# Kernel optimization log

Measured on AMD Instinct MI355X. Metric: run time of the kernel, lower is better.

## Reference

```python
import jax, jax.numpy as jnp
import numpy as np
from jax import lax

DH = 256   # d_hidden
NL = 8     # number of wavenet cells
K = 3      # kernel_size
DIN = 16   # d_lag + d_cov
DOUT = 1
T, B = 1024, 64


def setup_inputs() -> dict:
    key = jax.random.key(0)
    ks = jax.random.split(key, 20)
    s = 0.05
    inp = {
        "X_emb": jax.random.randint(ks[0], (T, B, 1), 0, 10),
        "X_cov": jax.random.normal(ks[1], (T, B, 8), jnp.float32),
        "X_lag": jax.random.normal(ks[2], (T, B, 8), jnp.float32),
        "y": jax.random.normal(ks[3], (T, B, DOUT), jnp.float32),
        "domain": jax.random.uniform(ks[4], (B, 4), jnp.float32),
        "up_w": jax.random.normal(ks[5], (DIN, DH), jnp.float32) * s,
        "up_b": jnp.zeros((DH,), jnp.float32),
        "conv_dil_w": jax.random.normal(ks[6], (NL, 2 * DH, DH, K), jnp.float32) * s,
        "conv_dil_b": jnp.zeros((NL, 2 * DH), jnp.float32),
        "skip_w": jax.random.normal(ks[7], (NL, 2 * DH, DH), jnp.float32) * s,
        "skip_b": jnp.zeros((NL, 2 * DH), jnp.float32),
        "fc_w": jax.random.normal(ks[8], (DH, DH), jnp.float32) * s,
        "fc_b": jnp.zeros((DH,), jnp.float32),
        "loc_w": jax.random.normal(ks[9], (DH, DOUT), jnp.float32) * s,
        "loc_b": jnp.zeros((DOUT,), jnp.float32),
        "scale_w": jax.random.normal(ks[10], (DH, DOUT), jnp.float32) * s,
        "scale_b": jnp.zeros((DOUT,), jnp.float32),
        "d_outputseqlen": 24,
    }
    return inp


def _causal_conv(h, w, b, dil):
    # h: [B, C, T], w: [O, C, K] -> causal (left-padded) dilated conv
    pad = (w.shape[-1] - 1) * dil
    y = lax.conv_general_dilated(h, w, window_strides=(1,), padding=[(pad, 0)],
                                 rhs_dilation=(dil,),
                                 dimension_numbers=("NCH", "OIH", "NCH"))
    return y + b[None, :, None]


def _forward(X_cov, X_lag, y, up_w, up_b, conv_dil_w, conv_dil_b,
             skip_w, skip_b, fc_w, fc_b, loc_w, loc_b, scale_w, scale_b,
             d_outputseqlen):
    t = X_lag.shape[0]
    h = jnp.concatenate([X_lag, X_cov[:t]], axis=-1) @ up_w + up_b  # [T,B,DH]
    h = jnp.transpose(h, (1, 2, 0))  # [B, DH, T]
    skip = jnp.zeros_like(h)
    for i in range(NL):
        fg = _causal_conv(h, conv_dil_w[i], conv_dil_b[i], 2 ** i)  # [B,2DH,T]
        f, g = jnp.split(fg, 2, axis=1)
        gated = jnp.tanh(f) * jax.nn.sigmoid(g)  # [B,DH,T]
        hs = jnp.einsum("oc,bct->bot", skip_w[i], gated) + skip_b[i][None, :, None]
        h_next, skip_next = jnp.split(hs, 2, axis=1)
        h = h + h_next
        skip = skip + skip_next
    feat = jnp.transpose(skip, (2, 0, 1))  # [T,B,DH]
    ff = jax.nn.relu(feat @ fc_w + fc_b)
    tail = ff[-d_outputseqlen:]
    loc = tail @ loc_w + loc_b
    scale = jax.nn.softplus(tail @ scale_w + scale_b) + 1e-6
    yt = y[-d_outputseqlen:]
    log_prob = (-0.5 * ((yt - loc) / scale) ** 2
                - jnp.log(scale) - 0.5 * np.log(2.0 * np.pi))
    loss_y = -jnp.mean(log_prob)
    total_loss = loss_y  # loss_d forced to 0 in the original forward
    return total_loss, loss_y, loc, scale


def reference(X_emb, X_cov, X_lag, y, domain, up_w, up_b, conv_dil_w,
              conv_dil_b, skip_w, skip_b, fc_w, fc_b, loc_w, loc_b,
              scale_w, scale_b, d_outputseqlen):
    # X_emb and domain are unused with d_emb=[] and loss_d hard-set to 0.
    return _forward(X_cov, X_lag, y, up_w, up_b, conv_dil_w, conv_dil_b,
                    skip_w, skip_b, fc_w, fc_b, loc_w, loc_b,
                    scale_w, scale_b, d_outputseqlen)
```

## Files before the change

kernel.cpp:

```cpp
#include <hip/hip_runtime.h>
#include <math.h>

static constexpr int TT = 1024, BB = 64, DHID = 256, NLAY = 8, OSL = 24;

typedef __attribute__((ext_vector_type(8))) short short8;
typedef __attribute__((ext_vector_type(4))) float f32x4;
typedef unsigned short u16;
typedef __attribute__((ext_vector_type(4))) unsigned short u16x4;
typedef unsigned int u32;

__device__ __forceinline__ u16 f2bf(float x) {
  u32 u = __float_as_uint(x);
  return (u16)((u + 0x7fffu + ((u >> 16) & 1u)) >> 16);
}

__device__ __forceinline__ void gll16(const u16* g, u16* l) {
  __builtin_amdgcn_global_load_lds((const __attribute__((address_space(1))) void*)g,
                                   (__attribute__((address_space(3))) void*)l, 16, 0, 0);
}

__global__ __launch_bounds__(256) void wprep(
    const float* __restrict__ cw, const float* __restrict__ sw,
    u16* __restrict__ wT, u16* __restrict__ swT)
{
  const int stride = gridDim.x * 256;
  for (int idx = blockIdx.x * 256 + threadIdx.x; idx < NLAY * 3 * 512 * 256; idx += stride) {
    const int c = idx & 255;
    const int o = (idx >> 8) & 511;
    const int lt = idx >> 17;
    const int tap = lt % 3, l = lt / 3;
    wT[idx] = f2bf(cw[((size_t)(l * 512 + o) * 256 + c) * 3 + tap]);
  }
  for (int idx = blockIdx.x * 256 + threadIdx.x; idx < NLAY * 512 * 256; idx += stride)
    swT[idx] = f2bf(sw[idx]);
}

__global__ __launch_bounds__(256) void up_kernel(
    const float* __restrict__ xlag, const float* __restrict__ xcov,
    const float* __restrict__ upw, const float* __restrict__ upb,
    float* __restrict__ h, u16* __restrict__ hb0)
{
  const int b  = blockIdx.y;
  const int t0 = blockIdx.x * 16;
  __shared__ float xs[16][17];
  {
    const int tl = threadIdx.x >> 4;
    const int j  = threadIdx.x & 15;
    const size_t base = ((size_t)(t0 + tl) * BB + b) * 8;
    xs[tl][j] = (j < 8) ? xlag[base + j] : xcov[base + (j - 8)];
  }
  __syncthreads();
  const int c = threadIdx.x;
  float uw[16];
#pragma unroll
  for (int j = 0; j < 16; ++j) uw[j] = upw[j * DHID + c];
  const float bias = upb[c];
#pragma unroll
  for (int tl = 0; tl < 16; ++tl) {
    float acc = bias;
#pragma unroll
    for (int j = 0; j < 16; ++j) acc = fmaf(xs[tl][j], uw[j], acc);
    const size_t idx = ((size_t)b * TT + t0 + tl) * DHID + c;
    h[idx]   = acc;
    hb0[idx] = f2bf(acc);
  }
}

__global__ __launch_bounds__(512, 4) void layer_fused(
    const u16* __restrict__ hbin, const u16* __restrict__ wT,
    const float* __restrict__ cb, const u16* __restrict__ swT,
    const float* __restrict__ sb, float* __restrict__ hf,
    u16* __restrict__ hbout, float* __restrict__ skipf,
    const int dil, const int tile0)
{
  __shared__ u16 As[512 * 32];
  __shared__ u16 Bs[64 * 32];
  __shared__ u16 gLDS[64 * 264];

  const int b    = blockIdx.y;
  const int tile = tile0 + blockIdx.x;
  const int t0   = tile * 64;
  const bool last = (tile == 15);
  const int tid = threadIdx.x, w = tid >> 6, lane = tid & 63;
  const int l16 = lane & 15, quad = lane >> 4;
  const u16* hb = hbin + (size_t)b * TT * DHID;

  f32x4 acc[4][4];
  const f32x4 zero = {0.f, 0.f, 0.f, 0.f};
#pragma unroll
  for (int m = 0; m < 4; ++m)
#pragma unroll
    for (int n = 0; n < 4; ++n) acc[m][n] = zero;

  for (int tap = 0; tap < 3; ++tap) {
    const int sh = (2 - tap) * dil;
    const u16* wtap = wT + (size_t)tap * 512 * 256;
    for (int kc = 0; kc < 8; ++kc) {
      const int c0 = kc * 32;
#pragma unroll
      for (int q = 0; q < 4; ++q) {
        const int lin = q * 512 + tid;
        gll16(wtap + (size_t)(lin >> 2) * 256 + c0 + (lin & 3) * 8,
              As + (size_t)(q * 512 + (tid & ~63)) * 8);
      }
      if (w < 4) {
        const int tl = 16 * w + (lane >> 2);
        gll16(hb + (size_t)(t0 - sh + tl) * 256 + c0 + (lane & 3) * 8,
              Bs + w * 512);
      }
      __syncthreads();
      short8 bfr[4], afr[4];
#pragma unroll
      for (int nt = 0; nt < 4; ++nt)
        bfr[nt] = *(const short8*)&Bs[(nt * 16 + l16) * 32 + quad * 8];
#pragma unroll
      for (int m = 0; m < 4; ++m) {
        const int o = ((m & 2) ? 256 : 0) + 32 * w + (m & 1) * 16 + l16;
        afr[m] = *(const short8*)&As[(size_t)o * 32 + quad * 8];
      }
#pragma unroll
      for (int m = 0; m < 4; ++m)
#pragma unroll
        for (int nt = 0; nt < 4; ++nt)
          acc[m][nt] = __builtin_amdgcn_mfma_f32_16x16x32_bf16(afr[m], bfr[nt], acc[m][nt], 0, 0, 0);
      __syncthreads();
    }
  }

#pragma unroll
  for (int mf = 0; mf < 2; ++mf) {
#pragma unroll
    for (int nt = 0; nt < 4; ++nt) {
      u16x4 pk;
#pragma unroll
      for (int r = 0; r < 4; ++r) {
        const int c = 32 * w + mf * 16 + quad * 4 + r;
        const float f = acc[mf][nt][r] + cb[c];
        const float g = acc[mf + 2][nt][r] + cb[256 + c];
        const float th = 2.f / (1.f + __expf(-2.f * f)) - 1.f;
        const float sg = 1.f / (1.f + __expf(-g));
        pk[r] = f2bf(th * sg);
      }
      *(u16x4*)&gLDS[(size_t)(nt * 16 + l16) * 264 + 32 * w + mf * 16 + quad * 4] = pk;
    }
  }
  __syncthreads();

#pragma unroll
  for (int m = 0; m < 4; ++m)
#pragma unroll
    for (int n = 0; n < 4; ++n) acc[m][n] = zero;

  const int nq = last ? 4 : 2;
  for (int kc = 0; kc < 8; ++kc) {
    const int c0 = kc * 32;
    for (int q = 0; q < nq; ++q) {
      const int lin = q * 512 + tid;
      gll16(swT + (size_t)(lin >> 2) * 256 + c0 + (lin & 3) * 8,
            As + (size_t)(q * 512 + (tid & ~63)) * 8);
    }
    __syncthreads();
    short8 bfr[4];
#pragma unroll
    for (int nt = 0; nt < 4; ++nt)
      bfr[nt] = *(const short8*)&gLDS[(size_t)(nt * 16 + l16) * 264 + c0 + quad * 8];
#pragma unroll
    for (int m = 0; m < 2; ++m) {
      const int o = 32 * w + m * 16 + l16;
      short8 a = *(const short8*)&As[(size_t)o * 32 + quad * 8];
#pragma unroll
      for (int nt = 0; nt < 4; ++nt)
        acc[m][nt] = __builtin_amdgcn_mfma_f32_16x16x32_bf16(a, bfr[nt], acc[m][nt], 0, 0, 0);
    }
    if (last) {
#pragma unroll
      for (int m = 2; m < 4; ++m) {
        const int o = 256 + 32 * w + (m & 1) * 16 + l16;
        short8 a = *(const short8*)&As[(size_t)o * 32 + quad * 8];
#pragma unroll
        for (int nt = 0; nt < 4; ++nt)
          acc[m][nt] = __builtin_amdgcn_mfma_f32_16x16x32_bf16(a, bfr[nt], acc[m][nt], 0, 0, 0);
      }
    }
    __syncthreads();
  }

#pragma unroll
  for (int mh = 0; mh < 2; ++mh) {
#pragma unroll
    for (int nt = 0; nt < 4; ++nt) {
      const int t  = t0 + nt * 16 + l16;
      const int c4 = 32 * w + mh * 16 + quad * 4;
      const size_t idx = ((size_t)b * TT + t) * DHID + c4;
      f32x4 hv = *(f32x4*)&hf[idx];
      u16x4 pk;
#pragma unroll
      for (int r = 0; r < 4; ++r) {
        const float v = hv[r] + acc[mh][nt][r] + sb[c4 + r];
        hv[r] = v;
        pk[r] = f2bf(v);
      }
      *(f32x4*)&hf[idx] = hv;
      *(u16x4*)&hbout[idx] = pk;
    }
  }
  if (last) {
#pragma unroll
    for (int mh = 0; mh < 2; ++mh) {
#pragma unroll
      for (int nt = 0; nt < 4; ++nt) {
        const int tl = nt * 16 + l16;
        const int c4 = 32 * w + mh * 16 + quad * 4;
        const size_t idx = ((size_t)b * 64 + tl) * DHID + c4;
        f32x4 sv = *(f32x4*)&skipf[idx];
#pragma unroll
        for (int r = 0; r < 4; ++r)
          sv[r] += acc[mh + 2][nt][r] + sb[256 + c4 + r];
        *(f32x4*)&skipf[idx] = sv;
      }
    }
  }
}

__global__ __launch_bounds__(256) void head_kernel(
    const float* __restrict__ skipf,
    const float* __restrict__ fcw, const float* __restrict__ fcb,
    const float* __restrict__ locw, const float* __restrict__ locb,
    const float* __restrict__ scw, const float* __restrict__ scb,
    float* __restrict__ out)
{
  const int tt = blockIdx.x;
  const int b  = blockIdx.y;
  const int tl = 40 + tt;
  const int c  = threadIdx.x;
  __shared__ float xs[DHID];
  xs[c] = skipf[((size_t)b * 64 + tl) * DHID + c];
  __syncthreads();
  float acc = fcb[c];
#pragma unroll 8
  for (int j = 0; j < DHID; ++j) acc = fmaf(xs[j], fcw[j * DHID + c], acc);
  const float ff = fmaxf(acc, 0.f);
  float pl = ff * locw[c];
  float ps = ff * scw[c];
#pragma unroll
  for (int off = 32; off > 0; off >>= 1) {
    pl += __shfl_down(pl, off);
    ps += __shfl_down(ps, off);
  }
  __shared__ float rl[4], rs[4];
  const int wid = threadIdx.x >> 6, lane = threadIdx.x & 63;
  if (lane == 0) { rl[wid] = pl; rs[wid] = ps; }
  __syncthreads();
  if (threadIdx.x == 0) {
    const float loc = rl[0] + rl[1] + rl[2] + rl[3] + locb[0];
    const float x   = rs[0] + rs[1] + rs[2] + rs[3] + scb[0];
    const float sp  = (x > 0.f) ? (x + log1pf(expf(-x))) : log1pf(expf(x));
    out[2 + tt * BB + b]            = loc;
    out[2 + OSL * BB + tt * BB + b] = sp + 1e-6f;
  }
}

__global__ __launch_bounds__(256) void loss_kernel(
    const float* __restrict__ y, float* __restrict__ out)
{
  float s = 0.f;
  for (int i = threadIdx.x; i < OSL * BB; i += 256) {
    const int tt = i >> 6, b = i & 63;
    const float loc = out[2 + i];
    const float sc  = out[2 + OSL * BB + i];
    const float yt  = y[(size_t)(TT - OSL + tt) * BB + b];
    const float z   = (yt - loc) / sc;
    s += -0.5f * z * z - logf(sc) - 0.9189385332046727f;
  }
#pragma unroll
  for (int off = 32; off > 0; off >>= 1) s += __shfl_down(s, off);
  __shared__ float r[4];
  if ((threadIdx.x & 63) == 0) r[threadIdx.x >> 6] = s;
  __syncthreads();
  if (threadIdx.x == 0) {
    const float loss = -(r[0] + r[1] + r[2] + r[3]) / (float)(OSL * BB);
    out[0] = loss;
    out[1] = loss;
  }
}

extern "C" void kernel_launch(void* const* d_in, const int* in_sizes, int n_in,
                              void* d_out, int out_size, void* d_ws, size_t ws_size,
                              hipStream_t stream) {
  (void)in_sizes; (void)n_in; (void)out_size; (void)ws_size;
  const float* X_cov  = (const float*)d_in[1];
  const float* X_lag  = (const float*)d_in[2];
  const float* y      = (const float*)d_in[3];
  const float* up_w   = (const float*)d_in[5];
  const float* up_b   = (const float*)d_in[6];
  const float* conv_w = (const float*)d_in[7];
  const float* conv_b = (const float*)d_in[8];
  const float* skip_w = (const float*)d_in[9];
  const float* skip_b = (const float*)d_in[10];
  const float* fc_w   = (const float*)d_in[11];
  const float* fc_b   = (const float*)d_in[12];
  const float* loc_w  = (const float*)d_in[13];
  const float* loc_b  = (const float*)d_in[14];
  const float* sc_w   = (const float*)d_in[15];
  const float* sc_b   = (const float*)d_in[16];

  float* hf    = (float*)d_ws;
  u16*   hb0   = (u16*)  ((char*)d_ws + 67108864);
  u16*   hb1   = (u16*)  ((char*)d_ws + 100663296);
  float* skipf = (float*)((char*)d_ws + 134217728);
  u16*   wT    = (u16*)  ((char*)d_ws + 138412032);
  u16*   swT   = (u16*)  ((char*)d_ws + 144703488);

  wprep<<<2048, 256, 0, stream>>>(conv_w, skip_w, wT, swT);
  hipMemsetAsync(skipf, 0, (size_t)BB * 64 * DHID * sizeof(float), stream);
  up_kernel<<<dim3(TT / 16, BB), 256, 0, stream>>>(X_lag, X_cov, up_w, up_b, hf, hb0);

  static const int Ptab[NLAY] = {4, 5, 6, 7, 8, 9, 11, 15};
  u16* hin = hb0;
  u16* hout = hb1;
  for (int i = 0; i < NLAY; ++i) {
    const int ntiles = 16 - Ptab[i];
    layer_fused<<<dim3(ntiles, BB), 512, 0, stream>>>(
        hin, wT + (size_t)i * 3 * 512 * 256, conv_b + i * 512,
        swT + (size_t)i * 512 * 256, skip_b + i * 512,
        hf, hout, skipf, 1 << i, Ptab[i]);
    u16* tmp = hin; hin = hout; hout = tmp;
  }

  head_kernel<<<dim3(OSL, BB), 256, 0, stream>>>(
      skipf, fc_w, fc_b, loc_w, loc_b, sc_w, sc_b, (float*)d_out);
  loss_kernel<<<1, 256, 0, stream>>>(y, (float*)d_out);
}
```

Measured before the change: 734.3 us.

## Double-buffer layer GEMM with two batches per 1024-thread block

The fused layer kernel now processes two batch elements per 1024-thread block, so each staged weight tile is reused across 128 time positions instead of 64. LDS staging is double-buffered across the 24 conv steps and the 8 skip steps, which removes one barrier per step and overlaps loads with MFMA work. The up-projection kernel also skips the first 192 timesteps, which the receptive-field pruning of the later layers never reads. The larger blocks cut occupancy and raise LDS use per block, and the grid has half as many blocks.

```diff
diff --git a/kernel.cpp b/kernel.cpp
--- a/kernel.cpp
+++ b/kernel.cpp
@@ -41,7 +41,7 @@
     float* __restrict__ h, u16* __restrict__ hb0)
 {
   const int b  = blockIdx.y;
-  const int t0 = blockIdx.x * 16;
+  const int t0 = 192 + blockIdx.x * 16;
   __shared__ float xs[16][17];
   {
     const int tl = threadIdx.x >> 4;
@@ -66,156 +66,172 @@
   }
 }
 
-__global__ __launch_bounds__(512, 4) void layer_fused(
+__global__ __launch_bounds__(1024) void layer_fused(
     const u16* __restrict__ hbin, const u16* __restrict__ wT,
-    const float* __restrict__ cb, const u16* __restrict__ swT,
+    const float* __restrict__ cb, const u16* __restrict__ swTl,
     const float* __restrict__ sb, float* __restrict__ hf,
     u16* __restrict__ hbout, float* __restrict__ skipf,
     const int dil, const int tile0)
 {
-  __shared__ u16 As[512 * 32];
-  __shared__ u16 Bs[64 * 32];
-  __shared__ u16 gLDS[64 * 264];
-
-  const int b    = blockIdx.y;
+  __shared__ u16 As[2][2048 * 8];
+  __shared__ u16 Bs[2][512 * 8];
+  __shared__ u16 gS[4096 * 8];
+
+  const int b0   = blockIdx.y * 2;
   const int tile = tile0 + blockIdx.x;
   const int t0   = tile * 64;
   const bool last = (tile == 15);
-  const int tid = threadIdx.x, w = tid >> 6, lane = tid & 63;
+  const int tid = threadIdx.x;
+  const int w = tid >> 6, lane = tid & 63;
   const int l16 = lane & 15, quad = lane >> 4;
-  const u16* hb = hbin + (size_t)b * TT * DHID;
-
-  f32x4 acc[4][4];
+  const u16* hbB = hbin + (size_t)b0 * TT * DHID;
+
+  f32x4 acc[2][8];
   const f32x4 zero = {0.f, 0.f, 0.f, 0.f};
 #pragma unroll
-  for (int m = 0; m < 4; ++m)
-#pragma unroll
-    for (int n = 0; n < 4; ++n) acc[m][n] = zero;
-
-  for (int tap = 0; tap < 3; ++tap) {
+  for (int m = 0; m < 2; ++m)
+#pragma unroll
+    for (int n = 0; n < 8; ++n) acc[m][n] = zero;
+
+  auto stageConv = [&](int buf, int tap, int kc) {
     const int sh = (2 - tap) * dil;
+    const int c0 = kc * 32;
     const u16* wtap = wT + (size_t)tap * 512 * 256;
-    for (int kc = 0; kc < 8; ++kc) {
-      const int c0 = kc * 32;
-#pragma unroll
-      for (int q = 0; q < 4; ++q) {
-        const int lin = q * 512 + tid;
-        gll16(wtap + (size_t)(lin >> 2) * 256 + c0 + (lin & 3) * 8,
-              As + (size_t)(q * 512 + (tid & ~63)) * 8);
-      }
-      if (w < 4) {
-        const int tl = 16 * w + (lane >> 2);
-        gll16(hb + (size_t)(t0 - sh + tl) * 256 + c0 + (lane & 3) * 8,
-              Bs + w * 512);
-      }
-      __syncthreads();
-      short8 bfr[4], afr[4];
-#pragma unroll
-      for (int nt = 0; nt < 4; ++nt)
-        bfr[nt] = *(const short8*)&Bs[(nt * 16 + l16) * 32 + quad * 8];
-#pragma unroll
-      for (int m = 0; m < 4; ++m) {
-        const int o = ((m & 2) ? 256 : 0) + 32 * w + (m & 1) * 16 + l16;
-        afr[m] = *(const short8*)&As[(size_t)o * 32 + quad * 8];
-      }
-#pragma unroll
-      for (int m = 0; m < 4; ++m)
-#pragma unroll
-        for (int nt = 0; nt < 4; ++nt)
-          acc[m][nt] = __builtin_amdgcn_mfma_f32_16x16x32_bf16(afr[m], bfr[nt], acc[m][nt], 0, 0, 0);
-      __syncthreads();
-    }
-  }
-
-#pragma unroll
-  for (int mf = 0; mf < 2; ++mf) {
-#pragma unroll
-    for (int nt = 0; nt < 4; ++nt) {
+#pragma unroll
+    for (int q = 0; q < 2; ++q) {
+      const int s = q * 1024 + tid;
+      const int p = s >> 9, o = s & 511;
+      gll16(wtap + (size_t)o * 256 + c0 + p * 8, As[buf] + (size_t)(s & ~63) * 8);
+    }
+    if (tid < 512) {
+      const int s = tid;
+      const int p = s >> 7, tp = s & 127;
+      gll16(hbB + ((size_t)(tp >> 6) * TT + (t0 - sh + (tp & 63))) * 256 + c0 + p * 8,
+            Bs[buf] + (size_t)(s & ~63) * 8);
+    }
+  };
+  auto stageSkip = [&](int buf, int kc) {
+    const int c0 = kc * 32;
+    if (!last) {
+      const int s = tid;
+      const int p = s >> 8, o = s & 255;
+      gll16(swTl + (size_t)o * 256 + c0 + p * 8, As[buf] + (size_t)(s & ~63) * 8);
+    } else {
+#pragma unroll
+      for (int q = 0; q < 2; ++q) {
+        const int s = q * 1024 + tid;
+        const int p = s >> 9, o = s & 511;
+        gll16(swTl + (size_t)o * 256 + c0 + p * 8, As[buf] + (size_t)(s & ~63) * 8);
+      }
+    }
+  };
+
+  stageConv(0, 0, 0);
+  __syncthreads();
+  for (int step = 0; step < 24; ++step) {
+    const int ns = step + 1;
+    if (ns < 24) stageConv(ns & 1, ns >> 3, ns & 7);
+    else         stageSkip(0, 0);
+    const u16* A = As[step & 1];
+    const u16* B = Bs[step & 1];
+    const short8 af0 = *(const short8*)&A[(size_t)(quad * 512 + 16 * w + l16) * 8];
+    const short8 af1 = *(const short8*)&A[(size_t)(quad * 512 + 256 + 16 * w + l16) * 8];
+#pragma unroll
+    for (int half = 0; half < 2; ++half) {
+      short8 bf[4];
+#pragma unroll
+      for (int j = 0; j < 4; ++j)
+        bf[j] = *(const short8*)&B[(size_t)(quad * 128 + 16 * (4 * half + j) + l16) * 8];
+#pragma unroll
+      for (int j = 0; j < 4; ++j) {
+        const int nt = 4 * half + j;
+        acc[0][nt] = __builtin_amdgcn_mfma_f32_16x16x32_bf16(af0, bf[j], acc[0][nt], 0, 0, 0);
+        acc[1][nt] = __builtin_amdgcn_mfma_f32_16x16x32_bf16(af1, bf[j], acc[1][nt], 0, 0, 0);
+      }
+    }
+    __syncthreads();
+  }
+
+  {
+    const int cpart = 2 * w + (quad >> 1);
+    const int e0 = 4 * (quad & 1);
+#pragma unroll
+    for (int nt = 0; nt < 8; ++nt) {
+      const int tp = 16 * nt + l16;
       u16x4 pk;
 #pragma unroll
       for (int r = 0; r < 4; ++r) {
-        const int c = 32 * w + mf * 16 + quad * 4 + r;
-        const float f = acc[mf][nt][r] + cb[c];
-        const float g = acc[mf + 2][nt][r] + cb[256 + c];
+        const int c = 16 * w + 4 * quad + r;
+        const float f = acc[0][nt][r] + cb[c];
+        const float g = acc[1][nt][r] + cb[256 + c];
         const float th = 2.f / (1.f + __expf(-2.f * f)) - 1.f;
         const float sg = 1.f / (1.f + __expf(-g));
         pk[r] = f2bf(th * sg);
       }
-      *(u16x4*)&gLDS[(size_t)(nt * 16 + l16) * 264 + 32 * w + mf * 16 + quad * 4] = pk;
-    }
-  }
-  __syncthreads();
-
-#pragma unroll
-  for (int m = 0; m < 4; ++m)
-#pragma unroll
-    for (int n = 0; n < 4; ++n) acc[m][n] = zero;
-
-  const int nq = last ? 4 : 2;
-  for (int kc = 0; kc < 8; ++kc) {
-    const int c0 = kc * 32;
-    for (int q = 0; q < nq; ++q) {
-      const int lin = q * 512 + tid;
-      gll16(swT + (size_t)(lin >> 2) * 256 + c0 + (lin & 3) * 8,
-            As + (size_t)(q * 512 + (tid & ~63)) * 8);
+      *(u16x4*)&gS[((size_t)cpart * 128 + tp) * 8 + e0] = pk;
+    }
+  }
+  __syncthreads();
+
+#pragma unroll
+  for (int m = 0; m < 2; ++m)
+#pragma unroll
+    for (int n = 0; n < 8; ++n) acc[m][n] = zero;
+
+  const int aStride = last ? 512 : 256;
+  for (int s2 = 0; s2 < 8; ++s2) {
+    if (s2 + 1 < 8) stageSkip((25 + s2) & 1, s2 + 1);
+    const u16* A = As[(24 + s2) & 1];
+    const short8 a0 = *(const short8*)&A[(size_t)(quad * aStride + 16 * w + l16) * 8];
+    short8 a1 = a0;
+    if (last) a1 = *(const short8*)&A[(size_t)(quad * 512 + 256 + 16 * w + l16) * 8];
+#pragma unroll
+    for (int half = 0; half < 2; ++half) {
+      short8 bf[4];
+#pragma unroll
+      for (int j = 0; j < 4; ++j)
+        bf[j] = *(const short8*)&gS[((size_t)(4 * s2 + quad) * 128 + 16 * (4 * half + j) + l16) * 8];
+#pragma unroll
+      for (int j = 0; j < 4; ++j) {
+        const int nt = 4 * half + j;
+        acc[0][nt] = __builtin_amdgcn_mfma_f32_16x16x32_bf16(a0, bf[j], acc[0][nt], 0, 0, 0);
+        if (last)
+          acc[1][nt] = __builtin_amdgcn_mfma_f32_16x16x32_bf16(a1, bf[j], acc[1][nt], 0, 0, 0);
+      }
     }
     __syncthreads();
-    short8 bfr[4];
-#pragma unroll
-    for (int nt = 0; nt < 4; ++nt)
-      bfr[nt] = *(const short8*)&gLDS[(size_t)(nt * 16 + l16) * 264 + c0 + quad * 8];
-#pragma unroll
-    for (int m = 0; m < 2; ++m) {
-      const int o = 32 * w + m * 16 + l16;
-      short8 a = *(const short8*)&As[(size_t)o * 32 + quad * 8];
-#pragma unroll
-      for (int nt = 0; nt < 4; ++nt)
-        acc[m][nt] = __builtin_amdgcn_mfma_f32_16x16x32_bf16(a, bfr[nt], acc[m][nt], 0, 0, 0);
-    }
-    if (last) {
-#pragma unroll
-      for (int m = 2; m < 4; ++m) {
-        const int o = 256 + 32 * w + (m & 1) * 16 + l16;
-        short8 a = *(const short8*)&As[(size_t)o * 32 + quad * 8];
-#pragma unroll
-        for (int nt = 0; nt < 4; ++nt)
-          acc[m][nt] = __builtin_amdgcn_mfma_f32_16x16x32_bf16(a, bfr[nt], acc[m][nt], 0, 0, 0);
-      }
-    }
-    __syncthreads();
-  }
-
-#pragma unroll
-  for (int mh = 0; mh < 2; ++mh) {
-#pragma unroll
-    for (int nt = 0; nt < 4; ++nt) {
-      const int t  = t0 + nt * 16 + l16;
-      const int c4 = 32 * w + mh * 16 + quad * 4;
-      const size_t idx = ((size_t)b * TT + t) * DHID + c4;
+  }
+
+  {
+    const int c4 = 16 * w + 4 * quad;
+#pragma unroll
+    for (int nt = 0; nt < 8; ++nt) {
+      const int tp = 16 * nt + l16;
+      const int bb = b0 + (tp >> 6);
+      const int t  = t0 + (tp & 63);
+      const size_t idx = ((size_t)bb * TT + t) * DHID + c4;
       f32x4 hv = *(f32x4*)&hf[idx];
       u16x4 pk;
 #pragma unroll
       for (int r = 0; r < 4; ++r) {
-        const float v = hv[r] + acc[mh][nt][r] + sb[c4 + r];
+        const float v = hv[r] + acc[0][nt][r] + sb[c4 + r];
         hv[r] = v;
         pk[r] = f2bf(v);
       }
       *(f32x4*)&hf[idx] = hv;
       *(u16x4*)&hbout[idx] = pk;
     }
-  }
-  if (last) {
-#pragma unroll
-    for (int mh = 0; mh < 2; ++mh) {
-#pragma unroll
-      for (int nt = 0; nt < 4; ++nt) {
-        const int tl = nt * 16 + l16;
-        const int c4 = 32 * w + mh * 16 + quad * 4;
-        const size_t idx = ((size_t)b * 64 + tl) * DHID + c4;
+    if (last) {
+#pragma unroll
+      for (int nt = 0; nt < 8; ++nt) {
+        const int tp = 16 * nt + l16;
+        const int bb = b0 + (tp >> 6);
+        const int tl = tp & 63;
+        const size_t idx = ((size_t)bb * 64 + tl) * DHID + c4;
         f32x4 sv = *(f32x4*)&skipf[idx];
 #pragma unroll
         for (int r = 0; r < 4; ++r)
-          sv[r] += acc[mh + 2][nt][r] + sb[256 + c4 + r];
+          sv[r] += acc[1][nt][r] + sb[256 + c4 + r];
         *(f32x4*)&skipf[idx] = sv;
       }
     }
@@ -313,14 +329,14 @@
 
   wprep<<<2048, 256, 0, stream>>>(conv_w, skip_w, wT, swT);
   hipMemsetAsync(skipf, 0, (size_t)BB * 64 * DHID * sizeof(float), stream);
-  up_kernel<<<dim3(TT / 16, BB), 256, 0, stream>>>(X_lag, X_cov, up_w, up_b, hf, hb0);
+  up_kernel<<<dim3(52, BB), 256, 0, stream>>>(X_lag, X_cov, up_w, up_b, hf, hb0);
 
   static const int Ptab[NLAY] = {4, 5, 6, 7, 8, 9, 11, 15};
   u16* hin = hb0;
   u16* hout = hb1;
   for (int i = 0; i < NLAY; ++i) {
     const int ntiles = 16 - Ptab[i];
-    layer_fused<<<dim3(ntiles, BB), 512, 0, stream>>>(
+    layer_fused<<<dim3(ntiles, BB / 2), 1024, 0, stream>>>(
         hin, wT + (size_t)i * 3 * 512 * 256, conv_b + i * 512,
         swT + (size_t)i * 512 * 256, skip_b + i * 512,
         hf, hout, skipf, 1 << i, Ptab[i]);
```

Result: slower. 1.226 ms (+67.0%).
